# Kernel optimization log

Hardware: AMD Instinct MI355X
Metric: run time of the kernel (lower is better)

## Reference

```python
import jax, jax.numpy as jnp
import numpy as np

DIM = 1024
HEADS = 16
DIM_HEAD = 64
INNER = HEADS * DIM_HEAD
SCALE = 8.0  # default scale in plain_cosine_sim_attention
EPS = 1e-5


def setup_inputs() -> dict:
    key = jax.random.key(0)
    ks = jax.random.split(key, 5)
    b, n = 2, 2048
    x = jax.random.normal(ks[0], (b, n, DIM), dtype=jnp.float32)
    ln_w = jnp.ones((DIM,), dtype=jnp.float32)
    ln_b = jnp.zeros((DIM,), dtype=jnp.float32)
    W_qkv = jax.random.normal(ks[1], (DIM, 3 * INNER), dtype=jnp.float32) * (DIM ** -0.5)
    W_out = jax.random.normal(ks[2], (INNER, DIM), dtype=jnp.float32) * (INNER ** -0.5)
    return {"x": x, "ln_w": ln_w, "ln_b": ln_b, "W_qkv": W_qkv, "W_out": W_out}


def _l2norm(t):
    return t / jnp.clip(jnp.linalg.norm(t, axis=-1, keepdims=True), 1e-12)


def reference(x, ln_w, ln_b, W_qkv, W_out):
    b, n, _ = x.shape
    # LayerNorm
    mu = jnp.mean(x, axis=-1, keepdims=True)
    var = jnp.var(x, axis=-1, keepdims=True)
    xn = (x - mu) * jax.lax.rsqrt(var + EPS) * ln_w + ln_b
    # QKV projection (no bias)
    qkv = xn @ W_qkv  # [b, n, 3*inner]
    q, k, v = jnp.split(qkv, 3, axis=-1)
    # [b, n, h*d] -> [b, h, n, d]
    def to_heads(t):
        return t.reshape(b, n, HEADS, DIM_HEAD).transpose(0, 2, 1, 3)
    q, k, v = to_heads(q), to_heads(k), to_heads(v)
    # cosine-sim attention: l2-normalize q, k then scaled dot product
    q = _l2norm(q)
    k = _l2norm(k)
    sim = jnp.einsum('bhid,bhjd->bhij', q, k) * SCALE
    # causal mask
    causal = jnp.tril(jnp.ones((n, n), dtype=bool))
    sim = jnp.where(causal, sim, jnp.finfo(sim.dtype).min)
    attn = jax.nn.softmax(sim, axis=-1)
    o = jnp.einsum('bhij,bhjd->bhid', attn, v)
    # [b, h, n, d] -> [b, n, h*d]
    o = o.transpose(0, 2, 1, 3).reshape(b, n, INNER)
    return o @ W_out
```

## Files before the change

kernel.cpp:

```cpp
#include <hip/hip_runtime.h>
#include <hip/hip_bf16.h>

typedef __attribute__((ext_vector_type(8))) short short8;
typedef __attribute__((ext_vector_type(4))) float floatx4;

__device__ __forceinline__ ushort f2bf(float f) {
    union { __hip_bfloat16 h; ushort u; } cv;
    cv.h = __float2bfloat16(f);
    return cv.u;
}
__device__ __forceinline__ float bf2f(ushort u) {
    union { ushort u; __hip_bfloat16 h; } cv;
    cv.u = u;
    return __bfloat162float(cv.h);
}
__device__ __forceinline__ ushort f2bf_rtz(float f) {
    union { float f; unsigned u; } cv;
    cv.f = f;
    return (ushort)(cv.u >> 16);
}

typedef __attribute__((address_space(1))) void* gas1_t;
typedef __attribute__((address_space(3))) void* las3_t;
__device__ __forceinline__ void cp16(const ushort* g, ushort* l) {
    __builtin_amdgcn_global_load_lds((gas1_t)(unsigned long long)g,
                                     (las3_t)(unsigned long long)l, 16, 0, 0);
}

__global__ __launch_bounds__(256) void prep_w_ln(const float* __restrict__ Wqkv,
                                                 const float* __restrict__ Wout,
                                                 ushort* __restrict__ WqkvT,
                                                 ushort* __restrict__ WoutT,
                                                 const float* __restrict__ x,
                                                 const float* __restrict__ lw,
                                                 const float* __restrict__ lb,
                                                 ushort* __restrict__ xn) {
    const int id = blockIdx.x;
    const int tid = threadIdx.x;
    if (id < 4096) {
        __shared__ float tile[32][33];
        int bx = id & 127, by = id >> 7;
        const float* in; ushort* out; int R = 1024, C;
        if (bx < 96) { in = Wqkv; out = WqkvT; C = 3072; }
        else { in = Wout; out = WoutT; C = 1024; bx -= 96; }
        int c0 = bx * 32, r0 = by * 32;
        int tx = tid & 31, ty = tid >> 5;
        for (int j = 0; j < 32; j += 8)
            tile[ty + j][tx] = in[(size_t)(r0 + ty + j) * C + c0 + tx];
        __syncthreads();
        for (int j = 0; j < 32; j += 8)
            out[(size_t)(c0 + ty + j) * R + r0 + tx] = f2bf(tile[tx][ty + j]);
    } else {
        int row = id - 4096;
        const float4* xr = (const float4*)(x + (size_t)row * 1024);
        float4 v = xr[tid];
        float s = v.x + v.y + v.z + v.w;
        float sq = v.x * v.x + v.y * v.y + v.z * v.z + v.w * v.w;
        for (int off = 32; off; off >>= 1) {
            s += __shfl_xor(s, off);
            sq += __shfl_xor(sq, off);
        }
        __shared__ float ls[4], lq[4];
        int wave = tid >> 6, lane = tid & 63;
        if (lane == 0) { ls[wave] = s; lq[wave] = sq; }
        __syncthreads();
        s = ls[0] + ls[1] + ls[2] + ls[3];
        sq = lq[0] + lq[1] + lq[2] + lq[3];
        float mu = s * (1.0f / 1024.0f);
        float var = sq * (1.0f / 1024.0f) - mu * mu;
        float rs = rsqrtf(var + 1e-5f);
        const float4* wr = (const float4*)lw;
        const float4* br = (const float4*)lb;
        float4 wv = wr[tid], bv = br[tid];
        ushort4 o;
        o.x = f2bf((v.x - mu) * rs * wv.x + bv.x);
        o.y = f2bf((v.y - mu) * rs * wv.y + bv.y);
        o.z = f2bf((v.z - mu) * rs * wv.z + bv.z);
        o.w = f2bf((v.w - mu) * rs * wv.w + bv.w);
        *(ushort4*)&xn[(size_t)row * 1024 + tid * 4] = o;
    }
}

__global__ __launch_bounds__(256) void gemm_qkv_fused(const ushort* __restrict__ A,
                                                      const ushort* __restrict__ Bt,
                                                      ushort* __restrict__ Qt,
                                                      ushort* __restrict__ Kt,
                                                      ushort* __restrict__ Vb) {
    __shared__ ushort smem[18432];
    const int K = 1024, T = 32;
    const int id = blockIdx.x;
    const int xcd = id & 7, r_ = id >> 3;
    const int bm = (xcd * 4 + r_ / 24) * 128;
    const int bn = r_ % 24;
    const int tid = threadIdx.x;
    const int wave = tid >> 6, lane = tid & 63;
    const int quad = lane >> 4, l15 = lane & 15;
    const int wm = (wave >> 1) * 64, wn = (wave & 1) * 64;

    const int s0 = tid, s1 = tid + 256;
    const int row0 = s0 >> 2, src0 = (s0 & 3) ^ (row0 & 3);
    const int row1 = s1 >> 2, src1 = (s1 & 3) ^ (row1 & 3);

    floatx4 acc[4][4];
    floatx4 z4 = {0.f, 0.f, 0.f, 0.f};
    for (int mi = 0; mi < 4; mi++)
        for (int ni = 0; ni < 4; ni++) acc[mi][ni] = z4;

    const ushort* Ap0 = A + (size_t)(bm + row0) * K + src0 * 8;
    const ushort* Ap1 = A + (size_t)(bm + row1) * K + src1 * 8;
    const ushort* Bp0 = Bt + (size_t)(bn * 128 + row0) * K + src0 * 8;
    const ushort* Bp1 = Bt + (size_t)(bn * 128 + row1) * K + src1 * 8;

    ushort* As = smem;
    ushort* Bs = smem + 8192;

    cp16(Ap0, &As[wave * 512]);
    cp16(Ap1, &As[2048 + wave * 512]);
    cp16(Bp0, &Bs[wave * 512]);
    cp16(Bp1, &Bs[2048 + wave * 512]);

    for (int t = 0; t < T; t++) {
        __syncthreads();
        if (t + 1 < T) {
            const int nb = (t + 1) & 1;
            const int k0n = (t + 1) << 5;
            cp16(Ap0 + k0n, &As[nb * 4096 + wave * 512]);
            cp16(Ap1 + k0n, &As[nb * 4096 + 2048 + wave * 512]);
            cp16(Bp0 + k0n, &Bs[nb * 4096 + wave * 512]);
            cp16(Bp1 + k0n, &Bs[nb * 4096 + 2048 + wave * 512]);
        }
        const ushort* Ab = As + (t & 1) * 4096;
        const ushort* Bb = Bs + (t & 1) * 4096;
        short8 af[4], bfr[4];
        for (int mi = 0; mi < 4; mi++) {
            int ra = wm + mi * 16 + l15;
            af[mi] = *(const short8*)&Ab[ra * 32 + ((quad ^ (ra & 3)) << 3)];
        }
        for (int ni = 0; ni < 4; ni++) {
            int rb = wn + ni * 16 + l15;
            bfr[ni] = *(const short8*)&Bb[rb * 32 + ((quad ^ (rb & 3)) << 3)];
        }
        for (int mi = 0; mi < 4; mi++)
            for (int ni = 0; ni < 4; ni++)
                acc[mi][ni] = __builtin_amdgcn_mfma_f32_16x16x32_bf16(
                    af[mi], bfr[ni], acc[mi][ni], 0, 0, 0);
    }

    const int col_base = bn * 128 + wn;
    const int type = col_base >> 10;
    const int h = (col_base & 1023) >> 6;
    const int row_base = bm + wm;

    if (type < 2) {
        ushort* dst = (type == 0) ? Qt : Kt;
        for (int mi = 0; mi < 4; mi++) {
            for (int r = 0; r < 4; r++) {
                float ss = 0.f;
                for (int ni = 0; ni < 4; ni++) ss += acc[mi][ni][r] * acc[mi][ni][r];
                for (int off = 1; off < 16; off <<= 1) ss += __shfl_xor(ss, off);
                float inv = rsqrtf(fmaxf(ss, 1e-24f));
                int rg = row_base + mi * 16 + quad * 4 + r;
                int bb = rg >> 11, n = rg & 2047;
                size_t orow = ((size_t)(bb * 16 + h) * 2048 + n) * 64;
                for (int ni = 0; ni < 4; ni++)
                    dst[orow + ni * 16 + l15] = f2bf(acc[mi][ni][r] * inv);
            }
        }
    } else {
        __syncthreads();
        ushort* tr = smem + wave * 4608;
        for (int mi = 0; mi < 4; mi++)
            for (int ni = 0; ni < 4; ni++)
                for (int r = 0; r < 4; r++) {
                    int row_l = mi * 16 + quad * 4 + r;
                    int col_l = ni * 16 + l15;
                    tr[col_l * 72 + row_l] = f2bf(acc[mi][ni][r]);
                }
        int bb = row_base >> 11, n0 = row_base & 2047;
        size_t vbase = ((size_t)(bb * 16 + h) * 32 + (n0 >> 6)) * 4096;
        const int dl = lane >> 3, nc = (lane & 7) * 8;
        for (int i = 0; i < 8; i++) {
            int d = dl + i * 8;
            short8 val = *(const short8*)&tr[d * 72 + nc];
            *(short8*)&Vb[vbase + (size_t)d * 64 + nc] = val;
        }
    }
}

__global__ __launch_bounds__(256) void gemm_out(const ushort* __restrict__ A,
                                                const ushort* __restrict__ Bt,
                                                float* __restrict__ C) {
    __shared__ ushort As[2][4096];
    __shared__ ushort Bs[2][4096];
    const int K = 1024, N = 1024;
    const int id = blockIdx.x;
    const int xcd = id & 7, r_ = id >> 3;
    const int bm = (xcd * 8 + (r_ >> 4)) * 64;
    const int bn = (r_ & 15) * 64;
    const int tid = threadIdx.x;
    const int wave = tid >> 6, lane = tid & 63;
    const int quad = lane >> 4, l15 = lane & 15;
    const int wm = (wave >> 1) * 32, wn = (wave & 1) * 32;

    const int ch0 = tid, ch1 = tid + 256;
    const int r0 = ch0 >> 3, sg0 = (ch0 & 7) ^ (r0 & 7);
    const int r1 = ch1 >> 3, sg1 = (ch1 & 7) ^ (r1 & 7);

    floatx4 acc[2][2];
    floatx4 z4 = {0.f, 0.f, 0.f, 0.f};
    for (int mi = 0; mi < 2; mi++)
        for (int ni = 0; ni < 2; ni++) acc[mi][ni] = z4;

    const ushort* Ap0 = A + (size_t)(bm + r0) * K + sg0 * 8;
    const ushort* Ap1 = A + (size_t)(bm + r1) * K + sg1 * 8;
    const ushort* Bp0 = Bt + (size_t)(bn + r0) * K + sg0 * 8;
    const ushort* Bp1 = Bt + (size_t)(bn + r1) * K + sg1 * 8;

    const int T = 16;
    cp16(Ap0, &As[0][wave * 512]);
    cp16(Ap1, &As[0][2048 + wave * 512]);
    cp16(Bp0, &Bs[0][wave * 512]);
    cp16(Bp1, &Bs[0][2048 + wave * 512]);

    for (int t = 0; t < T; t++) {
        __syncthreads();
        if (t + 1 < T) {
            const int nb = (t + 1) & 1;
            const int k0n = (t + 1) << 6;
            cp16(Ap0 + k0n, &As[nb][wave * 512]);
            cp16(Ap1 + k0n, &As[nb][2048 + wave * 512]);
            cp16(Bp0 + k0n, &Bs[nb][wave * 512]);
            cp16(Bp1 + k0n, &Bs[nb][2048 + wave * 512]);
        }
        const ushort* Ab = As[t & 1];
        const ushort* Bb = Bs[t & 1];
        short8 a0[2], a1[2], b0[2], b1[2];
        for (int mi = 0; mi < 2; mi++) {
            int ra = wm + mi * 16 + l15;
            a0[mi] = *(const short8*)&Ab[ra * 64 + ((quad ^ (ra & 7)) << 3)];
            a1[mi] = *(const short8*)&Ab[ra * 64 + (((quad + 4) ^ (ra & 7)) << 3)];
        }
        for (int ni = 0; ni < 2; ni++) {
            int rb = wn + ni * 16 + l15;
            b0[ni] = *(const short8*)&Bb[rb * 64 + ((quad ^ (rb & 7)) << 3)];
            b1[ni] = *(const short8*)&Bb[rb * 64 + (((quad + 4) ^ (rb & 7)) << 3)];
        }
        for (int mi = 0; mi < 2; mi++)
            for (int ni = 0; ni < 2; ni++) {
                acc[mi][ni] = __builtin_amdgcn_mfma_f32_16x16x32_bf16(
                    a0[mi], b0[ni], acc[mi][ni], 0, 0, 0);
                acc[mi][ni] = __builtin_amdgcn_mfma_f32_16x16x32_bf16(
                    a1[mi], b1[ni], acc[mi][ni], 0, 0, 0);
            }
    }
    for (int mi = 0; mi < 2; mi++)
        for (int ni = 0; ni < 2; ni++)
            for (int r = 0; r < 4; r++) {
                int row = bm + wm + mi * 16 + quad * 4 + r;
                int col = bn + wn + ni * 16 + l15;
                C[(size_t)row * N + col] = acc[mi][ni][r];
            }
}

#define LOG2E8 11.541560327111707f

__global__ __launch_bounds__(256) void flash_attn(const ushort* __restrict__ Qt,
                                                  const ushort* __restrict__ Kt,
                                                  const ushort* __restrict__ Vb,
                                                  ushort* __restrict__ O) {
    const int id = blockIdx.x;
    const int xcd = id & 7, r_ = id >> 3;
    const int bh = xcd + ((r_ & 3) << 3);
    const int u = r_ >> 2;
    const int s_ = u >> 3, g = u & 7;
    const int qt = (s_ == 0) ? g : (s_ == 1) ? (15 - g)
                 : (s_ == 2) ? (16 + g) : (31 - g);
    const int b = bh >> 4, h = bh & 15;
    const int tid = threadIdx.x;
    const int wave = tid >> 6, lane = tid & 63;
    const int quad = lane >> 4, l15 = lane & 15;

    __shared__ ushort Ks[2][64 * 64];
    __shared__ ushort Vs[64 * 64];
    __shared__ ushort Ps[4][16 * 64];

    const int ch0 = tid, ch1 = tid + 256;
    const int r0 = ch0 >> 3, sg0 = (ch0 & 7) ^ (r0 & 7);
    const int r1 = ch1 >> 3, sg1 = (ch1 & 7) ^ (r1 & 7);

    const ushort* Kp0 = Kt + ((size_t)bh * 2048 + r0) * 64 + sg0 * 8;
    const ushort* Kp1 = Kt + ((size_t)bh * 2048 + r1) * 64 + sg1 * 8;
    const ushort* Vp0 = Vb + (size_t)bh * 131072 + r0 * 64 + sg0 * 8;
    const ushort* Vp1 = Vb + (size_t)bh * 131072 + r1 * 64 + sg1 * 8;

    floatx4 z4 = {0.f, 0.f, 0.f, 0.f};

    const int q0 = qt * 64;
    const ushort* Qp = Qt + ((size_t)bh * 2048 + q0 + wave * 16 + l15) * 64;
    short8 qf0 = *(const short8*)(Qp + quad * 8);
    short8 qf1 = *(const short8*)(Qp + 32 + quad * 8);

    float rs_acc[4] = {0.f, 0.f, 0.f, 0.f};
    floatx4 o_acc[4];
    for (int ni = 0; ni < 4; ni++) o_acc[ni] = z4;

    cp16(Kp0, &Ks[0][wave * 512]);
    cp16(Kp1, &Ks[0][2048 + wave * 512]);
    short8 vA = *(const short8*)Vp0;
    short8 vB = *(const short8*)Vp1;

    for (int kt = 0; kt <= qt; kt++) {
        __syncthreads();
        *(short8*)&Vs[(unsigned)tid * 8] = vA;
        *(short8*)&Vs[(unsigned)(tid + 256) * 8] = vB;
        if (kt < qt) {
            const int nb2 = (kt + 1) & 1;
            const size_t to = (size_t)(kt + 1) * 4096;
            cp16(Kp0 + to, &Ks[nb2][wave * 512]);
            cp16(Kp1 + to, &Ks[nb2][2048 + wave * 512]);
            vA = *(const short8*)(Vp0 + to);
            vB = *(const short8*)(Vp1 + to);
        }
        const ushort* Kb = Ks[kt & 1];

        floatx4 s_acc[4];
        for (int ni = 0; ni < 4; ni++) s_acc[ni] = z4;
        for (int ni = 0; ni < 4; ni++) {
            int rb = ni * 16 + l15;
            short8 kf0 = *(const short8*)&Kb[rb * 64 + ((quad ^ (rb & 7)) << 3)];
            short8 kf1 = *(const short8*)&Kb[rb * 64 + (((quad + 4) ^ (rb & 7)) << 3)];
            s_acc[ni] = __builtin_amdgcn_mfma_f32_16x16x32_bf16(qf0, kf0, s_acc[ni], 0, 0, 0);
            s_acc[ni] = __builtin_amdgcn_mfma_f32_16x16x32_bf16(qf1, kf1, s_acc[ni], 0, 0, 0);
        }

        const bool diag = (kt == qt);
        for (int ni = 0; ni < 4; ni++) {
            const int col_loc = ni * 16 + l15;
            const int chnk = col_loc >> 3;
            for (int r = 0; r < 4; r++) {
                const int row_l = quad * 4 + r;
                float e = __builtin_amdgcn_exp2f(
                    fmaf(s_acc[ni][r], LOG2E8, -LOG2E8));
                if (diag && col_loc > wave * 16 + row_l) e = 0.f;
                rs_acc[r] += e;
                Ps[wave][row_l * 64 + (((chnk ^ (row_l & 7)) << 3) | (col_loc & 7))] =
                    f2bf_rtz(e);
            }
        }

        __syncthreads();

        short8 pa0 = *(const short8*)&Ps[wave][l15 * 64 + ((quad ^ (l15 & 7)) << 3)];
        short8 pa1 = *(const short8*)&Ps[wave][l15 * 64 + (((quad + 4) ^ (l15 & 7)) << 3)];
        for (int ni = 0; ni < 4; ni++) {
            int rv = ni * 16 + l15;
            short8 v0 = *(const short8*)&Vs[rv * 64 + ((quad ^ (rv & 7)) << 3)];
            short8 v1 = *(const short8*)&Vs[rv * 64 + (((quad + 4) ^ (rv & 7)) << 3)];
            o_acc[ni] = __builtin_amdgcn_mfma_f32_16x16x32_bf16(pa0, v0, o_acc[ni], 0, 0, 0);
            o_acc[ni] = __builtin_amdgcn_mfma_f32_16x16x32_bf16(pa1, v1, o_acc[ni], 0, 0, 0);
        }
    }

    for (int r = 0; r < 4; r++) {
        float rs = rs_acc[r];
        for (int off = 1; off < 16; off <<= 1) rs += __shfl_xor(rs, off);
        float inv = 1.0f / rs;
        int grow = q0 + wave * 16 + quad * 4 + r;
        size_t rowbase = ((size_t)b * 2048 + grow) * 1024 + h * 64;
        for (int ni = 0; ni < 4; ni++)
            O[rowbase + ni * 16 + l15] = f2bf(o_acc[ni][r] * inv);
    }
}

extern "C" void kernel_launch(void* const* d_in, const int* in_sizes, int n_in,
                              void* d_out, int out_size, void* d_ws, size_t ws_size,
                              hipStream_t stream) {
    const float* x = (const float*)d_in[0];
    const float* ln_w = (const float*)d_in[1];
    const float* ln_b = (const float*)d_in[2];
    const float* W_qkv = (const float*)d_in[3];
    const float* W_out = (const float*)d_in[4];

    char* w = (char*)d_ws;
    ushort* xn    = (ushort*)(w);
    ushort* obuf  = (ushort*)(w);
    ushort* WqkvT = (ushort*)(w + (8ull << 20));
    ushort* WoutT = (ushort*)(w + (14ull << 20));
    ushort* Vb    = (ushort*)(w + (16ull << 20));
    ushort* Qt    = (ushort*)(w + (24ull << 20));
    ushort* Kt    = (ushort*)(w + (32ull << 20));

    prep_w_ln<<<8192, 256, 0, stream>>>(W_qkv, W_out, WqkvT, WoutT, x, ln_w, ln_b, xn);
    gemm_qkv_fused<<<768, 256, 0, stream>>>(xn, WqkvT, Qt, Kt, Vb);
    flash_attn<<<1024, 256, 0, stream>>>(Qt, Kt, Vb, obuf);
    gemm_out<<<1024, 256, 0, stream>>>(obuf, WoutT, (float*)d_out);
}
```

Baseline: 174.8 us.

## Split long causal query tiles across two blocks with partial-sum combine kernel

Long causal query tiles (second half of sequence) are split across two blocks covering different key ranges, scheduled via a constant lookup table to balance per-block work. Those blocks write unnormalized fp32 partial outputs and row sums to scratch (the output buffer and a freed weight region), and a new combine kernel sums halves and normalizes. This shortens the critical-path tail of the attention kernel at the cost of an extra launch and extra memory traffic.

Result: slower. 182.7 us (+4.5%).

```diff
diff --git a/kernel.cpp b/kernel.cpp
--- a/kernel.cpp
+++ b/kernel.cpp
@@ -264,17 +264,34 @@
 
 #define LOG2E8 11.541560327111707f
 
+__constant__ unsigned FTAB[48] = {
+    0x0010000Fu, 0x00020001u, 0x000F001Du, 0x00120911u,
+    0x000D0019u, 0x00060005u, 0x000E001Au, 0x00080007u,
+    0x000F000Eu, 0x00130A12u, 0x0020101Fu, 0x00040003u,
+    0x00110910u, 0x001C0E1Bu, 0x00070006u, 0x000C0017u,
+    0x000E000Du, 0x000A0009u, 0x00030002u, 0x0010001Eu,
+    0x000F001Cu, 0x001A0D19u, 0x000D0018u, 0x00180C17u,
+    0x000B000Au, 0x0010001Fu, 0x000D000Cu, 0x001E0F1Du,
+    0x00050004u, 0x000C000Bu, 0x00190D18u, 0x00160B15u,
+    0x00090008u, 0x001F101Eu, 0x00150B14u, 0x00090010u,
+    0x000E001Bu, 0x000B0015u, 0x00140A13u, 0x000C0016u,
+    0x00010000u, 0x001D0F1Cu, 0x00090011u, 0x001B0E1Au,
+    0x00170C16u, 0x000A0013u, 0x000A0012u, 0x000B0014u
+};
+
 __global__ __launch_bounds__(256) void flash_attn(const ushort* __restrict__ Qt,
                                                   const ushort* __restrict__ Kt,
                                                   const ushort* __restrict__ Vb,
-                                                  ushort* __restrict__ O) {
+                                                  ushort* __restrict__ O,
+                                                  float* __restrict__ Opart,
+                                                  float* __restrict__ RSpart) {
     const int id = blockIdx.x;
     const int xcd = id & 7, r_ = id >> 3;
     const int bh = xcd + ((r_ & 3) << 3);
-    const int u = r_ >> 2;
-    const int s_ = u >> 3, g = u & 7;
-    const int qt = (s_ == 0) ? g : (s_ == 1) ? (15 - g)
-                 : (s_ == 2) ? (16 + g) : (31 - g);
+    const unsigned e = FTAB[r_ >> 2];
+    const int qt = e & 255;
+    const int ks = (e >> 8) & 255;
+    const int ke = (int)(e >> 16);
     const int b = bh >> 4, h = bh & 15;
     const int tid = threadIdx.x;
     const int wave = tid >> 6, lane = tid & 63;
@@ -304,16 +321,17 @@
     floatx4 o_acc[4];
     for (int ni = 0; ni < 4; ni++) o_acc[ni] = z4;
 
-    cp16(Kp0, &Ks[0][wave * 512]);
-    cp16(Kp1, &Ks[0][2048 + wave * 512]);
-    short8 vA = *(const short8*)Vp0;
-    short8 vB = *(const short8*)Vp1;
-
-    for (int kt = 0; kt <= qt; kt++) {
+    const size_t o0 = (size_t)ks * 4096;
+    cp16(Kp0 + o0, &Ks[ks & 1][wave * 512]);
+    cp16(Kp1 + o0, &Ks[ks & 1][2048 + wave * 512]);
+    short8 vA = *(const short8*)(Vp0 + o0);
+    short8 vB = *(const short8*)(Vp1 + o0);
+
+    for (int kt = ks; kt < ke; kt++) {
         __syncthreads();
         *(short8*)&Vs[(unsigned)tid * 8] = vA;
         *(short8*)&Vs[(unsigned)(tid + 256) * 8] = vB;
-        if (kt < qt) {
+        if (kt + 1 < ke) {
             const int nb2 = (kt + 1) & 1;
             const size_t to = (size_t)(kt + 1) * 4096;
             cp16(Kp0 + to, &Ks[nb2][wave * 512]);
@@ -339,12 +357,12 @@
             const int chnk = col_loc >> 3;
             for (int r = 0; r < 4; r++) {
                 const int row_l = quad * 4 + r;
-                float e = __builtin_amdgcn_exp2f(
+                float e2 = __builtin_amdgcn_exp2f(
                     fmaf(s_acc[ni][r], LOG2E8, -LOG2E8));
-                if (diag && col_loc > wave * 16 + row_l) e = 0.f;
-                rs_acc[r] += e;
+                if (diag && col_loc > wave * 16 + row_l) e2 = 0.f;
+                rs_acc[r] += e2;
                 Ps[wave][row_l * 64 + (((chnk ^ (row_l & 7)) << 3) | (col_loc & 7))] =
-                    f2bf_rtz(e);
+                    f2bf_rtz(e2);
             }
         }
 
@@ -361,15 +379,44 @@
         }
     }
 
-    for (int r = 0; r < 4; r++) {
-        float rs = rs_acc[r];
-        for (int off = 1; off < 16; off <<= 1) rs += __shfl_xor(rs, off);
-        float inv = 1.0f / rs;
-        int grow = q0 + wave * 16 + quad * 4 + r;
-        size_t rowbase = ((size_t)b * 2048 + grow) * 1024 + h * 64;
-        for (int ni = 0; ni < 4; ni++)
-            O[rowbase + ni * 16 + l15] = f2bf(o_acc[ni][r] * inv);
-    }
+    if (qt < 16) {
+        for (int r = 0; r < 4; r++) {
+            float rs = rs_acc[r];
+            for (int off = 1; off < 16; off <<= 1) rs += __shfl_xor(rs, off);
+            float inv = 1.0f / rs;
+            int grow = q0 + wave * 16 + quad * 4 + r;
+            size_t rowbase = ((size_t)b * 2048 + grow) * 1024 + h * 64;
+            for (int ni = 0; ni < 4; ni++)
+                O[rowbase + ni * 16 + l15] = f2bf(o_acc[ni][r] * inv);
+        }
+    } else {
+        const int half = (ks != 0) ? 1 : 0;
+        float* Oh = Opart + (size_t)half * 2097152
+                  + (size_t)(bh * 16 + (qt - 16)) * 4096;
+        float* RSp = RSpart + half * 32768 + (bh * 16 + (qt - 16)) * 64;
+        for (int r = 0; r < 4; r++) {
+            float rs = rs_acc[r];
+            for (int off = 1; off < 16; off <<= 1) rs += __shfl_xor(rs, off);
+            int rloc = wave * 16 + quad * 4 + r;
+            if (l15 == 0) RSp[rloc] = rs;
+            for (int ni = 0; ni < 4; ni++)
+                Oh[rloc * 64 + ni * 16 + l15] = o_acc[ni][r];
+        }
+    }
+}
+
+__global__ __launch_bounds__(256) void combine(const float* __restrict__ Opart,
+                                               const float* __restrict__ RSpart,
+                                               ushort* __restrict__ O) {
+    const int row = blockIdx.x * 4 + (threadIdx.x >> 6);
+    const int d = threadIdx.x & 63;
+    const float inv = 1.0f / (RSpart[row] + RSpart[32768 + row]);
+    const float o = Opart[(size_t)row * 64 + d]
+                  + Opart[2097152 + (size_t)row * 64 + d];
+    const int bh = row >> 10;
+    const int b = bh >> 4, h = bh & 15;
+    const int n = 1024 + (row & 1023);
+    O[((size_t)b * 2048 + n) * 1024 + h * 64 + d] = f2bf(o * inv);
 }
 
 extern "C" void kernel_launch(void* const* d_in, const int* in_sizes, int n_in,
@@ -389,9 +436,12 @@
     ushort* Vb    = (ushort*)(w + (16ull << 20));
     ushort* Qt    = (ushort*)(w + (24ull << 20));
     ushort* Kt    = (ushort*)(w + (32ull << 20));
+    float*  Opart  = (float*)d_out;
+    float*  RSpart = (float*)(w + (8ull << 20));
 
     prep_w_ln<<<8192, 256, 0, stream>>>(W_qkv, W_out, WqkvT, WoutT, x, ln_w, ln_b, xn);
     gemm_qkv_fused<<<768, 256, 0, stream>>>(xn, WqkvT, Qt, Kt, Vb);
-    flash_attn<<<1024, 256, 0, stream>>>(Qt, Kt, Vb, obuf);
+    flash_attn<<<1536, 256, 0, stream>>>(Qt, Kt, Vb, obuf, Opart, RSpart);
+    combine<<<8192, 256, 0, stream>>>(Opart, RSpart, obuf);
     gemm_out<<<1024, 256, 0, stream>>>(obuf, WoutT, (float*)d_out);
 }
```
